# Performance work log

Measured on AMD Instinct MI355X. Metric: run time of the kernel, lower is better.

The kernel has to match this reference:

```python
import jax, jax.numpy as jnp
import numpy as np
import math

HEADS = 16
D_MODEL = 1024
D_K = D_MODEL // HEADS


def setup_inputs() -> dict:
    key = jax.random.key(0)
    ks = jax.random.split(key, 11)
    B, S = 2, 2048
    s = 1.0 / math.sqrt(D_MODEL)
    return {
        "q": jax.random.normal(ks[0], (B, S, D_MODEL), jnp.float32),
        "k": jax.random.normal(ks[1], (B, S, D_MODEL), jnp.float32),
        "v": jax.random.normal(ks[2], (B, S, D_MODEL), jnp.float32),
        "Wq": jax.random.normal(ks[3], (D_MODEL, D_MODEL), jnp.float32) * s,
        "bq": jax.random.normal(ks[4], (D_MODEL,), jnp.float32) * s,
        "Wk": jax.random.normal(ks[5], (D_MODEL, D_MODEL), jnp.float32) * s,
        "bk": jax.random.normal(ks[6], (D_MODEL,), jnp.float32) * s,
        "Wv": jax.random.normal(ks[7], (D_MODEL, D_MODEL), jnp.float32) * s,
        "bv": jax.random.normal(ks[8], (D_MODEL,), jnp.float32) * s,
        "Wo": jax.random.normal(ks[9], (D_MODEL, D_MODEL), jnp.float32) * s,
        "bo": jax.random.normal(ks[10], (D_MODEL,), jnp.float32) * s,
    }


def reference(q, k, v, Wq, bq, Wk, bk, Wv, bv, Wo, bo):
    B, S, _ = q.shape
    # linear projections, split heads: [B, H, S, d_k]
    def proj(x, W, b):
        y = x @ W.T + b
        return y.reshape(B, -1, HEADS, D_K).transpose(0, 2, 1, 3)
    qh, kh, vh = proj(q, Wq, bq), proj(k, Wk, bk), proj(v, Wv, bv)
    # abs-modified scaled dot-product attention (no mask, eval -> no dropout)
    scores = jnp.abs(jnp.einsum("bhsd,bhtd->bhst", qh, kh) / math.sqrt(D_K))
    attn = jax.nn.softmax(scores, axis=-1)
    out = jnp.einsum("bhst,bhtd->bhsd", attn, vh)
    concat = out.transpose(0, 2, 1, 3).reshape(B, S, D_MODEL)
    return concat @ Wo.T + bo
```

## Files before the change

### kernel.cpp

```cpp
#include <hip/hip_runtime.h>

#define HEADS 16
#define DK 64
#define DM 1024
#define SEQ 2048
#define BATCH 2

using bf16x8 = __attribute__((ext_vector_type(8))) short;
using short4v = __attribute__((ext_vector_type(4))) short;
using f32x4 = __attribute__((ext_vector_type(4))) float;

static __device__ __forceinline__ short f2bf(float x) {
  union { float f; unsigned u; } c;
  c.f = x;
  unsigned r = (c.u + 0x7FFFu + ((c.u >> 16) & 1u)) >> 16;
  return (short)r;
}

static __device__ __forceinline__ void gload_lds16(const void* g, void* l) {
  __builtin_amdgcn_global_load_lds(
      (const __attribute__((address_space(1))) void*)g,
      (__attribute__((address_space(3))) void*)l, 16, 0, 0);
}

__global__ __launch_bounds__(256) void cvt7(
    const float* __restrict__ s0, const float* __restrict__ s1,
    const float* __restrict__ s2, const float* __restrict__ s3,
    const float* __restrict__ s4, const float* __restrict__ s5,
    const float* __restrict__ s6, short* d0, short* d1, short* d2, short* d3,
    short* d4, short* d5, short* d6) {
  const int y = blockIdx.y;
  const float* s;
  short* d;
  int n;
  switch (y) {
    case 0: s = s0; d = d0; n = BATCH * SEQ * DM; break;
    case 1: s = s1; d = d1; n = BATCH * SEQ * DM; break;
    case 2: s = s2; d = d2; n = BATCH * SEQ * DM; break;
    case 3: s = s3; d = d3; n = DM * DM; break;
    case 4: s = s4; d = d4; n = DM * DM; break;
    case 5: s = s5; d = d5; n = DM * DM; break;
    default: s = s6; d = d6; n = DM * DM; break;
  }
  const int n4 = n >> 2;
  const int stride = gridDim.x * 256;
  for (int i = blockIdx.x * 256 + threadIdx.x; i < n4; i += stride) {
    float4 v = ((const float4*)s)[i];
    short4v o;
    o.x = f2bf(v.x);
    o.y = f2bf(v.y);
    o.z = f2bf(v.z);
    o.w = f2bf(v.w);
    ((short4v*)d)[i] = o;
  }
}

__global__ __launch_bounds__(256) void proj_qkv(
    const short* __restrict__ Aq, const short* __restrict__ Ak,
    const short* __restrict__ Av, const short* __restrict__ Wq_,
    const short* __restrict__ Wk_, const short* __restrict__ Wv_,
    const float* __restrict__ bq, const float* __restrict__ bk,
    const float* __restrict__ bv, short* __restrict__ Qh,
    short* __restrict__ Kh, short* __restrict__ Vt) {
  __shared__ short smem[128 * 136];
  short* As = smem;
  short* Ws = smem + 8192;

  const int z = blockIdx.z;
  const short* A = z == 0 ? Aq : z == 1 ? Ak : Av;
  const short* W = z == 0 ? Wq_ : z == 1 ? Wk_ : Wv_;
  const float* bias = z == 0 ? bq : z == 1 ? bk : bv;
  short* C = z == 0 ? Qh : z == 1 ? Kh : Vt;
  const bool tr = (z == 2);

  const int tid = threadIdx.x;
  const int wave = tid >> 6, lane = tid & 63;
  const int quad = lane >> 4, l15 = lane & 15;
  const int n0 = blockIdx.x * 128, m0 = blockIdx.y * 128;
  const int mh = (wave & 1) * 64, nh = (wave >> 1) * 64;
  const int ldr = lane >> 3, ldc = lane & 7;

  f32x4 acc[4][4] = {};

  for (int k0 = 0; k0 < 1024; k0 += 64) {
    __syncthreads();
#pragma unroll
    for (int i = 0; i < 8; ++i) {
      int seg = wave * 8 + i;
      int r = (seg & 15) * 8 + ldr;
      int kb = ldc ^ (r & 7);
      if (seg < 16)
        gload_lds16(&A[(size_t)(m0 + r) * 1024 + k0 + kb * 8], &As[seg * 512]);
      else
        gload_lds16(&W[(size_t)(n0 + r) * 1024 + k0 + kb * 8],
                    &Ws[(seg - 16) * 512]);
    }
    __syncthreads();
#pragma unroll
    for (int ks = 0; ks < 2; ++ks) {
      bf16x8 a[4], b[4];
      int kb = ks * 4 + quad;
#pragma unroll
      for (int f = 0; f < 4; ++f) {
        int rm = mh + f * 16 + l15;
        int rn = nh + f * 16 + l15;
        a[f] = *(const bf16x8*)&As[rm * 64 + (kb ^ (rm & 7)) * 8];
        b[f] = *(const bf16x8*)&Ws[rn * 64 + (kb ^ (rn & 7)) * 8];
      }
#pragma unroll
      for (int mf = 0; mf < 4; ++mf)
#pragma unroll
        for (int nf = 0; nf < 4; ++nf)
          acc[mf][nf] = __builtin_amdgcn_mfma_f32_16x16x32_bf16(
              a[mf], b[nf], acc[mf][nf], 0, 0, 0);
    }
  }

  float bvv[4];
#pragma unroll
  for (int nf = 0; nf < 4; ++nf) bvv[nf] = bias[n0 + nh + nf * 16 + l15];

  __syncthreads();
  short* Cb = smem;

  if (!tr) {
    const float osc = (z == 0) ? 0.18033688011112042f : 1.0f;
#pragma unroll
    for (int mf = 0; mf < 4; ++mf)
#pragma unroll
      for (int nf = 0; nf < 4; ++nf)
#pragma unroll
        for (int r = 0; r < 4; ++r)
          Cb[(mh + mf * 16 + quad * 4 + r) * 136 + nh + nf * 16 + l15] =
              f2bf((acc[mf][nf][r] + bvv[nf]) * osc);
    __syncthreads();
#pragma unroll
    for (int j = 0; j < 8; ++j) {
      int cid = tid + 256 * j;
      int row = cid >> 4, cb = cid & 15;
      bf16x8 v = *(const bf16x8*)&Cb[row * 136 + cb * 8];
      int m = m0 + row, n = n0 + cb * 8;
      int b = m >> 11, s = m & (SEQ - 1), h = n >> 6, d = n & 63;
      *(bf16x8*)&C[((size_t)(b * HEADS + h) * SEQ + s) * DK + d] = v;
    }
  } else {
#pragma unroll
    for (int mf = 0; mf < 4; ++mf)
#pragma unroll
      for (int nf = 0; nf < 4; ++nf) {
        short4v p;
        p.x = f2bf(acc[mf][nf][0] + bvv[nf]);
        p.y = f2bf(acc[mf][nf][1] + bvv[nf]);
        p.z = f2bf(acc[mf][nf][2] + bvv[nf]);
        p.w = f2bf(acc[mf][nf][3] + bvv[nf]);
        *(short4v*)&Cb[(nh + nf * 16 + l15) * 136 + mh + mf * 16 + quad * 4] =
            p;
      }
    __syncthreads();
#pragma unroll
    for (int j = 0; j < 8; ++j) {
      int cid = tid + 256 * j;
      int row = cid >> 4, cb = cid & 15;
      bf16x8 v = *(const bf16x8*)&Cb[row * 136 + cb * 8];
      int n = n0 + row, m = m0 + cb * 8;
      int b = m >> 11, s = m & (SEQ - 1), h = n >> 6, d = n & 63;
      *(bf16x8*)&C[((size_t)(b * HEADS + h) * DK + d) * SEQ + s] = v;
    }
  }
}

__global__ __launch_bounds__(256) void proj_out(const short* __restrict__ A,
                                                const short* __restrict__ W,
                                                const float* __restrict__ bias,
                                                float* __restrict__ C) {
  __shared__ short smem[128 * 136];
  short* As = smem;
  short* Ws = smem + 8192;

  const int tid = threadIdx.x;
  const int wave = tid >> 6, lane = tid & 63;
  const int quad = lane >> 4, l15 = lane & 15;
  const int n0 = blockIdx.x * 128, m0 = blockIdx.y * 128;
  const int mh = (wave & 1) * 64, nh = (wave >> 1) * 64;
  const int ldr = lane >> 3, ldc = lane & 7;

  f32x4 acc[4][4] = {};

  for (int k0 = 0; k0 < 1024; k0 += 64) {
    __syncthreads();
#pragma unroll
    for (int i = 0; i < 8; ++i) {
      int seg = wave * 8 + i;
      int r = (seg & 15) * 8 + ldr;
      int kb = ldc ^ (r & 7);
      if (seg < 16)
        gload_lds16(&A[(size_t)(m0 + r) * 1024 + k0 + kb * 8], &As[seg * 512]);
      else
        gload_lds16(&W[(size_t)(n0 + r) * 1024 + k0 + kb * 8],
                    &Ws[(seg - 16) * 512]);
    }
    __syncthreads();
#pragma unroll
    for (int ks = 0; ks < 2; ++ks) {
      bf16x8 a[4], b[4];
      int kb = ks * 4 + quad;
#pragma unroll
      for (int f = 0; f < 4; ++f) {
        int rm = mh + f * 16 + l15;
        int rn = nh + f * 16 + l15;
        a[f] = *(const bf16x8*)&As[rm * 64 + (kb ^ (rm & 7)) * 8];
        b[f] = *(const bf16x8*)&Ws[rn * 64 + (kb ^ (rn & 7)) * 8];
      }
#pragma unroll
      for (int mf = 0; mf < 4; ++mf)
#pragma unroll
        for (int nf = 0; nf < 4; ++nf)
          acc[mf][nf] = __builtin_amdgcn_mfma_f32_16x16x32_bf16(
              a[mf], b[nf], acc[mf][nf], 0, 0, 0);
    }
  }

  float bvv[4];
#pragma unroll
  for (int nf = 0; nf < 4; ++nf) bvv[nf] = bias[n0 + nh + nf * 16 + l15];
#pragma unroll
  for (int mf = 0; mf < 4; ++mf)
#pragma unroll
    for (int nf = 0; nf < 4; ++nf)
#pragma unroll
      for (int r = 0; r < 4; ++r)
        C[(size_t)(m0 + mh + mf * 16 + quad * 4 + r) * 1024 + n0 + nh +
          nf * 16 + l15] = acc[mf][nf][r] + bvv[nf];
}

__global__ __launch_bounds__(256) void attn_mfma(const short* __restrict__ Qh,
                                                 const short* __restrict__ Kh,
                                                 const short* __restrict__ VtG,
                                                 short* __restrict__ concat) {
  __shared__ short Ksm[2][64 * 64];
  __shared__ short Vsm[2][64 * 64];
  __shared__ short Ps[128 * 64];

  const int tid = threadIdx.x;
  const int wave = tid >> 6, lane = tid & 63;
  const int quad = lane >> 4, l15 = lane & 15;
  const int bh = blockIdx.y;
  const int q0 = blockIdx.x * 128;
  const size_t base = (size_t)bh * SEQ * DK;
  const int ldr = lane >> 3, ldc = lane & 7;
  const int NT = SEQ / 64;
  const int row0 = wave * 32 + l15;
  const int rsw = (l15 & 7) << 1;

  bf16x8 qf[2][2];
#pragma unroll
  for (int mf = 0; mf < 2; ++mf)
#pragma unroll
    for (int ks = 0; ks < 2; ++ks)
      qf[mf][ks] =
          *(const bf16x8*)&Qh[base +
                              (size_t)(q0 + wave * 32 + mf * 16 + l15) * 64 +
                              ks * 32 + quad * 8];

  bf16x8 ones;
#pragma unroll
  for (int i = 0; i < 8; ++i) ones[i] = (short)0x3F80;

  f32x4 O[2][4] = {};
  f32x4 Lacc[2] = {};

  auto stage = [&](int kt, int buf) {
#pragma unroll
    for (int i = 0; i < 2; ++i) {
      int seg = wave * 2 + i;
      int r = seg * 8 + ldr;
      int kb = ldc ^ (r & 7);
      gload_lds16(&Kh[base + (size_t)(kt * 64 + r) * 64 + kb * 8],
                  &Ksm[buf][seg * 512]);
      gload_lds16(&VtG[base + (size_t)r * SEQ + kt * 64 + kb * 8],
                  &Vsm[buf][seg * 512]);
    }
  };

  stage(0, 0);
  __syncthreads();

  int cur = 0;
  for (int kt = 0; kt < NT; ++kt) {
    if (kt + 1 < NT) stage(kt + 1, cur ^ 1);

    const short* Ks = Ksm[cur];
    const short* Vs = Vsm[cur];

    f32x4 sf[2][4] = {};
#pragma unroll
    for (int ks = 0; ks < 2; ++ks) {
      bf16x8 kfr[4];
      int kb = ks * 4 + quad;
#pragma unroll
      for (int kf = 0; kf < 4; ++kf) {
        int n = kf * 16 + l15;
        kfr[kf] = *(const bf16x8*)&Ks[n * 64 + ((kb ^ (n & 7)) << 3)];
      }
#pragma unroll
      for (int kf = 0; kf < 4; ++kf)
#pragma unroll
        for (int mf = 0; mf < 2; ++mf)
          sf[mf][kf] = __builtin_amdgcn_mfma_f32_16x16x32_bf16(
              kfr[kf], qf[mf][ks], sf[mf][kf], 0, 0, 0);
    }

#pragma unroll
    for (int mf = 0; mf < 2; ++mf)
#pragma unroll
      for (int kf = 0; kf < 4; ++kf) {
        short4v p;
#pragma unroll
        for (int r = 0; r < 4; ++r)
          p[r] = f2bf(__builtin_amdgcn_exp2f(fabsf(sf[mf][kf][r])));
        *(short4v*)&Ps[(row0 + mf * 16) * 64 + (((kf * 4 + quad) ^ rsw) << 2)] =
            p;
      }
    __threadfence_block();

#pragma unroll
    for (int ks = 0; ks < 2; ++ks) {
      int kb = ks * 4 + quad;
      bf16x8 av[2];
#pragma unroll
      for (int mf = 0; mf < 2; ++mf)
        av[mf] = *(const bf16x8*)&Ps[(row0 + mf * 16) * 64 +
                                     (((ks * 8 + quad * 2) ^ rsw) << 2)];
      bf16x8 bvf[4];
#pragma unroll
      for (int nf = 0; nf < 4; ++nf) {
        int d = nf * 16 + l15;
        bvf[nf] = *(const bf16x8*)&Vs[d * 64 + ((kb ^ (d & 7)) << 3)];
      }
#pragma unroll
      for (int mf = 0; mf < 2; ++mf) {
#pragma unroll
        for (int nf = 0; nf < 4; ++nf)
          O[mf][nf] = __builtin_amdgcn_mfma_f32_16x16x32_bf16(
              av[mf], bvf[nf], O[mf][nf], 0, 0, 0);
        Lacc[mf] = __builtin_amdgcn_mfma_f32_16x16x32_bf16(av[mf], ones,
                                                           Lacc[mf], 0, 0, 0);
      }
    }

    __syncthreads();
    cur ^= 1;
  }

  float inv_[2][4];
#pragma unroll
  for (int mf = 0; mf < 2; ++mf)
#pragma unroll
    for (int r = 0; r < 4; ++r) inv_[mf][r] = 1.f / Lacc[mf][r];

#pragma unroll
  for (int mf = 0; mf < 2; ++mf)
#pragma unroll
    for (int nf = 0; nf < 4; ++nf)
#pragma unroll
      for (int r = 0; r < 4; ++r) {
        int rw = wave * 32 + mf * 16 + quad * 4 + r;
        int d = nf * 16 + l15;
        Ps[rw * 64 + (((d >> 3) ^ (rw & 7)) << 3) + (d & 7)] =
            f2bf(O[mf][nf][r] * inv_[mf][r]);
      }
  __syncthreads();
  const int b = bh >> 4, h = bh & 15;
#pragma unroll
  for (int j = 0; j < 4; ++j) {
    int cid = tid + 256 * j;
    int rw = cid >> 3, g = cid & 7;
    bf16x8 v = *(const bf16x8*)&Ps[rw * 64 + ((g ^ (rw & 7)) << 3)];
    *(bf16x8*)&concat[((size_t)(b * SEQ + q0 + rw)) * DM + h * 64 + g * 8] = v;
  }
}

extern "C" void kernel_launch(void* const* d_in, const int* in_sizes, int n_in,
                              void* d_out, int out_size, void* d_ws,
                              size_t ws_size, hipStream_t stream) {
  const float* q = (const float*)d_in[0];
  const float* k = (const float*)d_in[1];
  const float* v = (const float*)d_in[2];
  const float* Wq = (const float*)d_in[3];
  const float* bq = (const float*)d_in[4];
  const float* Wk = (const float*)d_in[5];
  const float* bk = (const float*)d_in[6];
  const float* Wv = (const float*)d_in[7];
  const float* bv = (const float*)d_in[8];
  const float* Wo = (const float*)d_in[9];
  const float* bo = (const float*)d_in[10];

  short* ws = (short*)d_ws;
  const size_t T4 = (size_t)BATCH * SEQ * DM;
  const size_t T1 = (size_t)DM * DM;
  short* qb = ws;
  short* kb_ = ws + T4;
  short* vb = ws + 2 * T4;
  short* Wqb = ws + 3 * T4;
  short* Wkb = Wqb + T1;
  short* Wvb = Wqb + 2 * T1;
  short* Wob = Wqb + 3 * T1;
  short* Qh = Wqb + 4 * T1;
  short* Kh = Qh + T4;
  short* VtG = Qh + 2 * T4;
  short* cc = Qh + 3 * T4;

  cvt7<<<dim3(1024, 7), 256, 0, stream>>>(q, k, v, Wq, Wk, Wv, Wo, qb, kb_, vb,
                                          Wqb, Wkb, Wvb, Wob);

  proj_qkv<<<dim3(DM / 128, (BATCH * SEQ) / 128, 3), 256, 0, stream>>>(
      qb, kb_, vb, Wqb, Wkb, Wvb, bq, bk, bv, Qh, Kh, VtG);

  attn_mfma<<<dim3(SEQ / 128, BATCH * HEADS), 256, 0, stream>>>(Qh, Kh, VtG,
                                                                cc);

  proj_out<<<dim3(DM / 128, (BATCH * SEQ) / 128), 256, 0, stream>>>(
      cc, Wob, bo, (float*)d_out);
}
```

Before: 238.0 us.

## Keep softmax probabilities in registers by permuting K rows to match MFMA layout

Reorders which K rows each lane loads (a row permutation plus a new LDS swizzle), so the S accumulator layout lines up directly with the A-operand layout of the PV MFMA. This removes the LDS round trip for P (the store, fence and reload) and the Ps shared buffer. The epilogue now reuses the K buffer for staging. It also adds s_setprio around the MFMA blocks to favour matrix issue across waves. The risk is subtle index errors in the permutation, plus extra register pressure from holding P fragments.

```diff
diff --git a/kernel.cpp b/kernel.cpp
--- a/kernel.cpp
+++ b/kernel.cpp
@@ -239,7 +239,6 @@
                                                  short* __restrict__ concat) {
   __shared__ short Ksm[2][64 * 64];
   __shared__ short Vsm[2][64 * 64];
-  __shared__ short Ps[128 * 64];
 
   const int tid = threadIdx.x;
   const int wave = tid >> 6, lane = tid & 63;
@@ -249,8 +248,6 @@
   const size_t base = (size_t)bh * SEQ * DK;
   const int ldr = lane >> 3, ldc = lane & 7;
   const int NT = SEQ / 64;
-  const int row0 = wave * 32 + l15;
-  const int rsw = (l15 & 7) << 1;
 
   bf16x8 qf[2][2];
 #pragma unroll
@@ -269,15 +266,20 @@
   f32x4 O[2][4] = {};
   f32x4 Lacc[2] = {};
 
+  int krow[4];
+#pragma unroll
+  for (int kf = 0; kf < 4; ++kf)
+    krow[kf] = 32 * (kf >> 1) + 8 * (l15 >> 2) + 4 * (kf & 1) + (l15 & 3);
+
   auto stage = [&](int kt, int buf) {
 #pragma unroll
     for (int i = 0; i < 2; ++i) {
       int seg = wave * 2 + i;
       int r = seg * 8 + ldr;
-      int kb = ldc ^ (r & 7);
-      gload_lds16(&Kh[base + (size_t)(kt * 64 + r) * 64 + kb * 8],
+      int kswz = (r & 7) ^ (((r >> 3) & 3) << 1);
+      gload_lds16(&Kh[base + (size_t)(kt * 64 + r) * 64 + (ldc ^ kswz) * 8],
                   &Ksm[buf][seg * 512]);
-      gload_lds16(&VtG[base + (size_t)r * SEQ + kt * 64 + kb * 8],
+      gload_lds16(&VtG[base + (size_t)r * SEQ + kt * 64 + (ldc ^ (r & 7)) * 8],
                   &Vsm[buf][seg * 512]);
     }
   };
@@ -299,53 +301,55 @@
       int kb = ks * 4 + quad;
 #pragma unroll
       for (int kf = 0; kf < 4; ++kf) {
-        int n = kf * 16 + l15;
-        kfr[kf] = *(const bf16x8*)&Ks[n * 64 + ((kb ^ (n & 7)) << 3)];
-      }
+        int n = krow[kf];
+        int kswz = (n & 7) ^ (((n >> 3) & 3) << 1);
+        kfr[kf] = *(const bf16x8*)&Ks[n * 64 + ((kb ^ kswz) << 3)];
+      }
+      __builtin_amdgcn_s_setprio(1);
 #pragma unroll
       for (int kf = 0; kf < 4; ++kf)
 #pragma unroll
         for (int mf = 0; mf < 2; ++mf)
           sf[mf][kf] = __builtin_amdgcn_mfma_f32_16x16x32_bf16(
               kfr[kf], qf[mf][ks], sf[mf][kf], 0, 0, 0);
-    }
-
+      __builtin_amdgcn_s_setprio(0);
+    }
+
+    bf16x8 pa[2][2];
 #pragma unroll
     for (int mf = 0; mf < 2; ++mf)
 #pragma unroll
-      for (int kf = 0; kf < 4; ++kf) {
-        short4v p;
-#pragma unroll
-        for (int r = 0; r < 4; ++r)
-          p[r] = f2bf(__builtin_amdgcn_exp2f(fabsf(sf[mf][kf][r])));
-        *(short4v*)&Ps[(row0 + mf * 16) * 64 + (((kf * 4 + quad) ^ rsw) << 2)] =
-            p;
-      }
-    __threadfence_block();
+      for (int ks = 0; ks < 2; ++ks) {
+        bf16x8 t;
+#pragma unroll
+        for (int half = 0; half < 2; ++half)
+#pragma unroll
+          for (int r = 0; r < 4; ++r)
+            t[half * 4 + r] = f2bf(
+                __builtin_amdgcn_exp2f(fabsf(sf[mf][2 * ks + half][r])));
+        pa[mf][ks] = t;
+      }
 
 #pragma unroll
     for (int ks = 0; ks < 2; ++ks) {
       int kb = ks * 4 + quad;
-      bf16x8 av[2];
-#pragma unroll
-      for (int mf = 0; mf < 2; ++mf)
-        av[mf] = *(const bf16x8*)&Ps[(row0 + mf * 16) * 64 +
-                                     (((ks * 8 + quad * 2) ^ rsw) << 2)];
       bf16x8 bvf[4];
 #pragma unroll
       for (int nf = 0; nf < 4; ++nf) {
         int d = nf * 16 + l15;
         bvf[nf] = *(const bf16x8*)&Vs[d * 64 + ((kb ^ (d & 7)) << 3)];
       }
+      __builtin_amdgcn_s_setprio(1);
 #pragma unroll
       for (int mf = 0; mf < 2; ++mf) {
 #pragma unroll
         for (int nf = 0; nf < 4; ++nf)
           O[mf][nf] = __builtin_amdgcn_mfma_f32_16x16x32_bf16(
-              av[mf], bvf[nf], O[mf][nf], 0, 0, 0);
-        Lacc[mf] = __builtin_amdgcn_mfma_f32_16x16x32_bf16(av[mf], ones,
+              pa[mf][ks], bvf[nf], O[mf][nf], 0, 0, 0);
+        Lacc[mf] = __builtin_amdgcn_mfma_f32_16x16x32_bf16(pa[mf][ks], ones,
                                                            Lacc[mf], 0, 0, 0);
       }
+      __builtin_amdgcn_s_setprio(0);
     }
 
     __syncthreads();
@@ -358,6 +362,7 @@
 #pragma unroll
     for (int r = 0; r < 4; ++r) inv_[mf][r] = 1.f / Lacc[mf][r];
 
+  short* Es = (short*)Ksm;
 #pragma unroll
   for (int mf = 0; mf < 2; ++mf)
 #pragma unroll
@@ -366,7 +371,7 @@
       for (int r = 0; r < 4; ++r) {
         int rw = wave * 32 + mf * 16 + quad * 4 + r;
         int d = nf * 16 + l15;
-        Ps[rw * 64 + (((d >> 3) ^ (rw & 7)) << 3) + (d & 7)] =
+        Es[rw * 64 + (((d >> 3) ^ (rw & 7)) << 3) + (d & 7)] =
             f2bf(O[mf][nf][r] * inv_[mf][r]);
       }
   __syncthreads();
@@ -375,7 +380,7 @@
   for (int j = 0; j < 4; ++j) {
     int cid = tid + 256 * j;
     int rw = cid >> 3, g = cid & 7;
-    bf16x8 v = *(const bf16x8*)&Ps[rw * 64 + ((g ^ (rw & 7)) << 3)];
+    bf16x8 v = *(const bf16x8*)&Es[rw * 64 + ((g ^ (rw & 7)) << 3)];
     *(bf16x8*)&concat[((size_t)(b * SEQ + q0 + rw)) * DM + h * 64 + g * 8] = v;
   }
 }
```

Measured after the change: 236.4 us. Within noise of the previous version (-0.6%).
